# Performance work log

Hardware: AMD Instinct MI355X
Metric: run time of the kernel (lower is better)

Reference implementation:

```python
import jax, jax.numpy as jnp
import numpy as np

B, T, C = 2, 2048, 2048
N_HEAD, D_HEAD = 16, 128

def setup_inputs() -> dict:
    key = jax.random.key(0)
    k1, k2, k3 = jax.random.split(key, 3)
    x = jax.random.normal(k1, (B, T, C), dtype=jnp.float32)
    # lecun-normal-ish scaling for kernels
    W_attn = jax.random.normal(k2, (C, 3 * C), dtype=jnp.float32) * (1.0 / np.sqrt(C))
    W_proj = jax.random.normal(k3, (C, C), dtype=jnp.float32) * (1.0 / np.sqrt(C))
    return {"x": x, "W_attn": W_attn, "W_proj": W_proj}

def reference(x, W_attn, W_proj):
    Bx, Tx, Cx = x.shape
    # fused qkv projection: (B,T,C) @ (C,3C)
    qkv = x @ W_attn
    q, k, v = jnp.split(qkv, 3, axis=-1)
    # (B, H, T, Dh)
    q = q.reshape(Bx, Tx, N_HEAD, D_HEAD).transpose(0, 2, 1, 3)
    k = k.reshape(Bx, Tx, N_HEAD, D_HEAD).transpose(0, 2, 1, 3)
    v = v.reshape(Bx, Tx, N_HEAD, D_HEAD).transpose(0, 2, 1, 3)
    scale = 1.0 / jnp.sqrt(jnp.asarray(D_HEAD, dtype=x.dtype))
    att = jnp.einsum('bhqd,bhkd->bhqk', q, k) * scale  # (B,H,T,T)
    causal_mask = jnp.tril(jnp.ones((Tx, Tx), dtype=jnp.bool_))[None, None]
    att = jnp.where(causal_mask, att, -jnp.inf)
    att = jax.nn.softmax(att, axis=-1)
    y = jnp.einsum('bhqk,bhkd->bhqd', att, v)
    y = y.transpose(0, 2, 1, 3).reshape(Bx, Tx, Cx)
    return y @ W_proj
```

## Files before the change

kernel.cpp:

```cpp
#include <hip/hip_runtime.h>
#include <hip/hip_bf16.h>
#include <stdint.h>

#define AS1 __attribute__((address_space(1)))
#define AS3 __attribute__((address_space(3)))

typedef __bf16 bf16_t;
typedef __bf16 bf16x8 __attribute__((ext_vector_type(8)));
typedef float f32x4 __attribute__((ext_vector_type(4)));
typedef float f32x16 __attribute__((ext_vector_type(16)));

static constexpr int Bsz = 2, T = 2048, Cdim = 2048, NH = 16, DH = 128;
static constexpr int M  = Bsz * T;
static constexpr int N1 = 3 * Cdim;
static constexpr int K1 = Cdim;

__device__ __forceinline__ unsigned short f2bf(float f) {
  unsigned u = __float_as_uint(f);
  u += 0x7fffu + ((u >> 16) & 1u);
  return (unsigned short)(u >> 16);
}

__device__ __forceinline__ void gload_lds16(const bf16_t* g, void* l) {
  __builtin_amdgcn_global_load_lds((AS1 const void*)g, (AS3 void*)l, 16, 0, 0);
}

__device__ __forceinline__ float ex2(float x) {
  float r; asm("v_exp_f32 %0, %1" : "=v"(r) : "v"(x)); return r;
}
__device__ __forceinline__ unsigned pk2(float a, float b) {
  unsigned r; asm("v_cvt_pk_bf16_f32 %0, %1, %2" : "=v"(r) : "v"(a), "v"(b)); return r;
}

__global__ __launch_bounds__(256) void preamble_kernel(const float* __restrict__ x,
                                                       const float* __restrict__ Wa,
                                                       const float* __restrict__ Wp,
                                                       unsigned short* __restrict__ xb,
                                                       unsigned short* __restrict__ WaT,
                                                       unsigned short* __restrict__ WpT) {
  __shared__ float tile[32][33];
  const int blk = blockIdx.x;
  const int tid = threadIdx.x;
  if (blk < 8192) {
    int i = blk * 1024 + tid * 4;
    float4 v = *(const float4*)(x + i);
    ushort4 o;
    o.x = f2bf(v.x); o.y = f2bf(v.y); o.z = f2bf(v.z); o.w = f2bf(v.w);
    *(ushort4*)(xb + i) = o;
    return;
  }
  const float* in;
  unsigned short* out;
  int Nn, bi;
  if (blk < 20480) { in = Wa; out = WaT; Nn = N1;   bi = blk - 8192;  }
  else             { in = Wp; out = WpT; Nn = Cdim; bi = blk - 20480; }
  const int ntiles = Nn >> 5;
  const int n0 = (bi % ntiles) * 32, k0 = (bi / ntiles) * 32;
  const int tx = tid & 31, ty = tid >> 5;
#pragma unroll
  for (int i = 0; i < 32; i += 8)
    tile[ty + i][tx] = in[(size_t)(k0 + ty + i) * Nn + n0 + tx];
  __syncthreads();
#pragma unroll
  for (int i = 0; i < 32; i += 8)
    out[(size_t)(n0 + ty + i) * K1 + k0 + tx] = f2bf(tile[tx][ty + i]);
}

__global__ __launch_bounds__(512, 2) void gemm_q(const bf16_t* __restrict__ A,
                                                 const bf16_t* __restrict__ BT,
                                                 void* __restrict__ Cp,
                                                 int Nn, int Kk) {
  constexpr int SLOT = 32768;
  __shared__ __align__(16) char ldsmem[3 * SLOT];
  char* ldsb = ldsmem;

  const int tid = threadIdx.x;
  const int lane = tid & 63;
  const int wid = tid >> 6;
  const int lq = lane & 15, lk = lane >> 4;
  const int wr = wid >> 2, wc = wid & 3;

  const int bid = blockIdx.x;
  const int xcd = bid & 7;
  const int j = bid >> 3;
  const int r = j & 15, s5 = j >> 4;
  const int tn = s5 * 8 + (r & 7);
  const int tm = xcd * 2 + (r >> 3);

  f32x4 acc[8][4] = {};

  int aoff[8], boff[4];
#pragma unroll
  for (int m = 0; m < 8; ++m) {
    int row = wr * 128 + m * 16 + lq;
    aoff[m] = row * 64 + ((lk * 16) ^ (((row >> 1) & 3) << 4));
  }
#pragma unroll
  for (int n = 0; n < 4; ++n) {
    int brow = wc * 64 + n * 16 + lq;
    boff[n] = 16384 + brow * 64 + ((lk * 16) ^ (((brow >> 1) & 3) << 4));
  }

  const int pA0 = tid * 16;
  const int ar0 = pA0 >> 6;
  const int ac0 = (pA0 & 63) ^ (((ar0 >> 1) & 3) << 4);
  const bf16_t* Ags0 = A + (size_t)(tm * 256 + ar0) * Kk + (ac0 >> 1);
  const int pA1 = 8192 + tid * 16;
  const int ar1 = pA1 >> 6;
  const int ac1 = (pA1 & 63) ^ (((ar1 >> 1) & 3) << 4);
  const bf16_t* Ags1 = A + (size_t)(tm * 256 + ar1) * Kk + (ac1 >> 1);
  const bf16_t* Bgs0 = BT + (size_t)(tn * 256 + ar0) * Kk + (ac0 >> 1);
  const bf16_t* Bgs1 = BT + (size_t)(tn * 256 + ar1) * Kk + (ac1 >> 1);

  auto stage = [&](int kt, int slot) {
    char* db = ldsb + slot * SLOT;
    gload_lds16(Ags0 + (size_t)kt * 32, db + tid * 16);
    gload_lds16(Ags1 + (size_t)kt * 32, db + 8192 + tid * 16);
    gload_lds16(Bgs0 + (size_t)kt * 32, db + 16384 + tid * 16);
    gload_lds16(Bgs1 + (size_t)kt * 32, db + 24576 + tid * 16);
  };

  const int nk = Kk >> 5;

  stage(0, 0); stage(1, 1);
  asm volatile("s_waitcnt vmcnt(4)" ::: "memory");
  __builtin_amdgcn_s_barrier();

#define QTILE(KT, SLOT0, SLOT2, STAGE_EN, VM)                                    \
  {                                                                              \
    const char* sb = ldsb + (SLOT0) * SLOT;                                      \
    bf16x8 af[8], bfv[4];                                                        \
    _Pragma("unroll") for (int m = 0; m < 8; ++m)                                \
      af[m] = *(const bf16x8*)(sb + aoff[m]);                                    \
    _Pragma("unroll") for (int n = 0; n < 4; ++n)                                \
      bfv[n] = *(const bf16x8*)(sb + boff[n]);                                   \
    if (STAGE_EN) stage((KT) + 2, (SLOT2));                                      \
    _Pragma("unroll") for (int m = 0; m < 8; ++m)                                \
      _Pragma("unroll") for (int n = 0; n < 4; ++n)                              \
        acc[m][n] =                                                              \
            __builtin_amdgcn_mfma_f32_16x16x32_bf16(af[m], bfv[n], acc[m][n], 0, 0, 0); \
    asm volatile("s_waitcnt vmcnt(" #VM ")" ::: "memory");                       \
    __builtin_amdgcn_s_barrier();                                                \
  }

  {
    int c0 = 0;
    for (int kt = 0; kt < nk - 2; ++kt) {
      const int c2 = (c0 >= 1) ? (c0 - 1) : (c0 + 2);
      QTILE(kt, c0, c2, 1, 4);
      c0 = (c0 >= 2) ? 0 : (c0 + 1);
    }
    QTILE(nk - 2, c0, 0, 0, 0);
    c0 = (c0 >= 2) ? 0 : (c0 + 1);
    QTILE(nk - 1, c0, 0, 0, 0);
  }
#undef QTILE

  if (tn >= 16) {
    unsigned short* q16 = (unsigned short*)Cp;
#pragma unroll
    for (int m = 0; m < 8; ++m)
#pragma unroll
      for (int n = 0; n < 4; ++n) {
        int row = tm * 256 + wr * 128 + m * 16 + lk * 4;
        int b_ = row >> 11, t0 = row & 2047;
        int c = tn * 256 - 4096 + wc * 64 + n * 16 + lq;
        ushort4 o;
        o.x = f2bf(acc[m][n][0]); o.y = f2bf(acc[m][n][1]);
        o.z = f2bf(acc[m][n][2]); o.w = f2bf(acc[m][n][3]);
        *(ushort4*)(q16 + (size_t)(b_ * 2048 + c) * N1 + 4096 + t0) = o;
      }
  } else {
#pragma unroll
    for (int m = 0; m < 8; ++m)
#pragma unroll
      for (int n = 0; n < 4; ++n)
#pragma unroll
        for (int r2 = 0; r2 < 4; ++r2) {
          int row = tm * 256 + wr * 128 + m * 16 + lk * 4 + r2;
          int col = tn * 256 + wc * 64 + n * 16 + lq;
          ((unsigned short*)Cp)[(size_t)row * Nn + col] = f2bf(acc[m][n][r2]);
        }
  }
}

template <int MODE>
__global__ __launch_bounds__(512, 4) void gemm_p3(const bf16_t* __restrict__ A,
                                                  const bf16_t* __restrict__ BT,
                                                  void* __restrict__ Cp,
                                                  int Nn, int Kk) {
  constexpr int SLOT = 24576;
  __shared__ __align__(16) char ldsmem[3 * SLOT];
  char* ldsb = ldsmem;

  const int tid = threadIdx.x;
  const int wid = tid >> 6, lane = tid & 63;
  const int lq = lane & 15, lk = lane >> 4;
  const int wr = wid >> 2, wc = wid & 3;

  const int bid = blockIdx.x;
  const int xcd = bid & 7;
  const int j = bid >> 3;
  const int r = j & 31, s5 = j >> 5;
  const int tn = s5 * 8 + (r & 7);
  const int tm = xcd * 4 + (r >> 3);

  f32x4 acc[4][4] = {};

  int aoff[4], boff[4];
#pragma unroll
  for (int m = 0; m < 4; ++m) {
    int row = wr * 64 + m * 16 + lq;
    aoff[m] = row * 64 + ((lk * 16) ^ (((row >> 1) & 3) << 4));
  }
#pragma unroll
  for (int n = 0; n < 4; ++n) {
    int brow = wc * 64 + n * 16 + lq;
    boff[n] = 8192 + brow * 64 + ((lk * 16) ^ (((brow >> 1) & 3) << 4));
  }

  const int pA = wid * 1024 + lane * 16;
  const int arow = pA >> 6;
  const int acsw = (pA & 63) ^ (((arow >> 1) & 3) << 4);
  const bf16_t* Ags = A + (size_t)(tm * 128 + arow) * Kk + (acsw >> 1);

  const int pB0 = wid * 1024 + lane * 16;
  const int brow0 = pB0 >> 6;
  const int bcsw0 = (pB0 & 63) ^ (((brow0 >> 1) & 3) << 4);
  const bf16_t* Bgs0 = BT + (size_t)(tn * 256 + brow0) * Kk + (bcsw0 >> 1);

  const int pB1 = 8192 + wid * 1024 + lane * 16;
  const int brow1 = pB1 >> 6;
  const int bcsw1 = (pB1 & 63) ^ (((brow1 >> 1) & 3) << 4);
  const bf16_t* Bgs1 = BT + (size_t)(tn * 256 + brow1) * Kk + (bcsw1 >> 1);

  const int ldsA = wid * 1024;
  const int ldsB0 = 8192 + wid * 1024;
  const int ldsB1 = 16384 + wid * 1024;

  auto stage = [&](int kt, int slot) {
    char* db = ldsb + slot * SLOT;
    gload_lds16(Ags + (size_t)kt * 32, db + ldsA);
    gload_lds16(Bgs0 + (size_t)kt * 32, db + ldsB0);
    gload_lds16(Bgs1 + (size_t)kt * 32, db + ldsB1);
  };

  const int nk = Kk >> 5;

  stage(0, 0); stage(1, 1);
  asm volatile("s_waitcnt vmcnt(3)" ::: "memory");
  __builtin_amdgcn_s_barrier();

#define TILE_BODY(KT, SLOT0, SLOT2, STAGE_EN, VM)                                \
  {                                                                              \
    __builtin_amdgcn_sched_barrier(0);                                           \
    const char* sb = ldsb + (SLOT0) * SLOT;                                      \
    bf16x8 af[4], bfv[4];                                                        \
    _Pragma("unroll") for (int m = 0; m < 4; ++m)                                \
      af[m] = *(const bf16x8*)(sb + aoff[m]);                                    \
    _Pragma("unroll") for (int n = 0; n < 4; ++n)                                \
      bfv[n] = *(const bf16x8*)(sb + boff[n]);                                   \
    if (STAGE_EN) stage((KT) + 2, (SLOT2));                                      \
    __builtin_amdgcn_sched_barrier(0);                                           \
    __builtin_amdgcn_s_barrier();                                                \
    asm volatile("s_waitcnt lgkmcnt(0)" ::: "memory");                           \
    __builtin_amdgcn_sched_barrier(0);                                           \
    __builtin_amdgcn_s_setprio(1);                                               \
    _Pragma("unroll") for (int m = 0; m < 4; ++m)                                \
      _Pragma("unroll") for (int n = 0; n < 4; ++n)                              \
        acc[m][n] =                                                              \
            __builtin_amdgcn_mfma_f32_16x16x32_bf16(af[m], bfv[n], acc[m][n], 0, 0, 0); \
    __builtin_amdgcn_s_setprio(0);                                               \
    __builtin_amdgcn_sched_barrier(0);                                           \
    asm volatile("s_waitcnt vmcnt(" #VM ")" ::: "memory");                       \
    __builtin_amdgcn_s_barrier();                                                \
  }

  {
    int c0 = 0;
    for (int kt = 0; kt < nk - 2; ++kt) {
      const int c2 = (c0 >= 1) ? (c0 - 1) : (c0 + 2);
      TILE_BODY(kt, c0, c2, 1, 3);
      c0 = (c0 >= 2) ? 0 : (c0 + 1);
    }
    TILE_BODY(nk - 2, c0, 0, 0, 0);
    c0 = (c0 >= 2) ? 0 : (c0 + 1);
    TILE_BODY(nk - 1, c0, 0, 0, 0);
  }
#undef TILE_BODY

#pragma unroll
  for (int m = 0; m < 4; ++m)
#pragma unroll
    for (int n = 0; n < 4; ++n)
#pragma unroll
      for (int r2 = 0; r2 < 4; ++r2) {
        int row = tm * 128 + wr * 64 + m * 16 + lk * 4 + r2;
        int col = tn * 256 + wc * 64 + n * 16 + lq;
        if (MODE == 1)
          ((unsigned short*)Cp)[(size_t)row * Nn + col] = f2bf(acc[m][n][r2]);
        else
          ((float*)Cp)[(size_t)row * Nn + col] = acc[m][n][r2];
      }
}

__global__ __launch_bounds__(512, 1) void attn_kernel(const bf16_t* __restrict__ qkv,
                                                      unsigned short* __restrict__ y) {
  __shared__ __align__(16) char lds[98304];
  const int tid = threadIdx.x;
  const int wid = tid >> 6, lane = tid & 63;
  const int l31 = lane & 31, hi = lane >> 5;
  const int hi16 = hi << 4;
  const int bh = blockIdx.x;
  const int g = blockIdx.y;
  const int b = bh >> 4, h = bh & 15;
  const float SC2 = 0.12751879868954096f;

  const int grp = (wid < 4) ? g : (15 - g);
  const int qlo = grp * 128 + (wid & 3) * 32;
  const int qidx = qlo + l31;
  const int nt = 2 * (15 - g) + 2;
  const size_t rowbase = (size_t)(b * T) * N1;

  bf16x8 qf[8];
  {
    const bf16_t* Qg = qkv + rowbase + (size_t)qidx * N1 + h * DH + hi * 8;
#pragma unroll
    for (int kk = 0; kk < 8; ++kk) qf[kk] = *(const bf16x8*)(Qg + kk * 16);
  }

  const bf16_t* Kg0 = qkv + rowbase + Cdim + h * DH;
  const bf16_t* Vg0 = qkv + (size_t)(b * 2048 + h * DH) * N1 + 2 * Cdim;
  const int p0 = wid * 1024 + lane * 16;
  const int p1 = 8192 + wid * 1024 + lane * 16;
  const int kr0 = p0 >> 8, kr1 = p1 >> 8;
  const bf16_t* KsA = Kg0 + (size_t)kr0 * N1 + ((((p0 & 255) ^ ((kr0 & 15) << 4))) >> 1);
  const bf16_t* KsB = Kg0 + (size_t)kr1 * N1 + ((((p1 & 255) ^ ((kr1 & 15) << 4))) >> 1);
  const int vr0 = p0 >> 7, vr1 = p1 >> 7;
  const bf16_t* VsA = Vg0 + (size_t)vr0 * N1 + ((((p0 & 127) ^ ((vr0 & 7) << 4))) >> 1);
  const bf16_t* VsB = Vg0 + (size_t)vr1 * N1 + ((((p1 & 127) ^ ((vr1 & 7) << 4))) >> 1);
  const int dstoff = wid * 1024;

  auto stage = [&](int tt, int slot) {
    char* Kd = lds + slot * 32768;
    char* Vd = Kd + 16384;
    const size_t ko = (size_t)(tt * 64) * N1;
    const int vo = tt * 64;
    gload_lds16(KsA + ko, Kd + dstoff);
    gload_lds16(KsB + ko, Kd + 8192 + dstoff);
    gload_lds16(VsA + vo, Vd + dstoff);
    gload_lds16(VsB + vo, Vd + 8192 + dstoff);
  };

  f32x16 oacc[4] = {};
  float mrow = -1e30f, lrow = 0.f;

  stage(0, 0); stage(1, 1);
  asm volatile("s_waitcnt vmcnt(4)" ::: "memory");
  __builtin_amdgcn_s_barrier();

  int cs = 0;
  for (int t = 0; t < nt; ++t) {
    const int kv0 = t * 64;
    if (t + 2 < nt) {
      const int s2 = (cs >= 1) ? (cs - 1) : (cs + 2);
      stage(t + 2, s2);
    }

    if (kv0 <= qlo + 31) {
      f32x16 s0 = {}, s1 = {};
      {
        const char* Kb = lds + cs * 32768;
        const char* krow0 = Kb + l31 * 256;
        const char* krow1 = Kb + (32 + l31) * 256;
        const int sw0 = (l31 & 15) << 4;
#pragma unroll
        for (int kk = 0; kk < 8; ++kk) {
          bf16x8 kf0 = *(const bf16x8*)(krow0 + ((kk * 32 + hi16) ^ sw0));
          bf16x8 kf1 = *(const bf16x8*)(krow1 + ((kk * 32 + hi16) ^ sw0));
          s0 = __builtin_amdgcn_mfma_f32_32x32x16_bf16(kf0, qf[kk], s0, 0, 0, 0);
          s1 = __builtin_amdgcn_mfma_f32_32x32x16_bf16(kf1, qf[kk], s1, 0, 0, 0);
        }
      }
      float sv[32];
#pragma unroll
      for (int r = 0; r < 16; ++r) { sv[r] = s0[r]; sv[16 + r] = s1[r]; }
      if (kv0 + 63 > qlo) {
#pragma unroll
        for (int r = 0; r < 16; ++r) {
          const int roff = (r & 3) + 8 * (r >> 2);
          if (kv0 + roff + 4 * hi > qidx) sv[r] = -1e30f;
          if (kv0 + 32 + roff + 4 * hi > qidx) sv[16 + r] = -1e30f;
        }
      }
      float mx = sv[0];
#pragma unroll
      for (int i = 1; i < 32; ++i) mx = fmaxf(mx, sv[i]);
      mx = fmaxf(mx, __shfl_xor(mx, 32));
      const float mn = fmaxf(mrow, mx);
      const float osc = ex2((mrow - mn) * SC2);
      mrow = mn;
      const float mn2 = mn * SC2;
#pragma unroll
      for (int db = 0; db < 4; ++db) oacc[db] *= osc;
      float srow = 0.f;
#pragma unroll
      for (int i = 0; i < 32; ++i) {
        float p = ex2(fmaf(sv[i], SC2, -mn2));
        sv[i] = p;
        srow += p;
      }
      srow += __shfl_xor(srow, 32);
      lrow = lrow * osc + srow;
      bf16x8 pb[4];
#pragma unroll
      for (int s4 = 0; s4 < 4; ++s4) {
        const int base = (s4 >> 1) * 16 + (s4 & 1) * 8;
        unsigned x0 = pk2(sv[base + 0], sv[base + 1]);
        unsigned x1 = pk2(sv[base + 2], sv[base + 3]);
        unsigned y0 = pk2(sv[base + 4], sv[base + 5]);
        unsigned y1 = pk2(sv[base + 6], sv[base + 7]);
        unsigned e0 = (unsigned)__shfl_xor((int)(hi ? x0 : y0), 32);
        unsigned e1 = (unsigned)__shfl_xor((int)(hi ? x1 : y1), 32);
        union { unsigned u[4]; bf16x8 v; } pbu;
        pbu.u[0] = hi ? e0 : x0;
        pbu.u[1] = hi ? e1 : x1;
        pbu.u[2] = hi ? y0 : e0;
        pbu.u[3] = hi ? y1 : e1;
        pb[s4] = pbu.v;
      }
      {
        const char* Vb = lds + cs * 32768 + 16384;
#pragma unroll
        for (int db = 0; db < 4; ++db) {
          const int vrow = db * 32 + l31;
          const char* vr = Vb + vrow * 128;
          const int swv = (vrow & 7) << 4;
#pragma unroll
          for (int s4 = 0; s4 < 4; ++s4) {
            bf16x8 vf = *(const bf16x8*)(vr + ((s4 * 32 + hi16) ^ swv));
            oacc[db] = __builtin_amdgcn_mfma_f32_32x32x16_bf16(vf, pb[s4], oacc[db], 0, 0, 0);
          }
        }
      }
    }

    asm volatile("s_waitcnt vmcnt(4)" ::: "memory");
    __builtin_amdgcn_s_barrier();
    cs = (cs >= 2) ? 0 : (cs + 1);
  }

  const float inv = 1.0f / lrow;
  char* eb = lds + wid * 8192;
#pragma unroll
  for (int db = 0; db < 4; ++db)
#pragma unroll
    for (int r = 0; r < 16; ++r) {
      const int d = db * 32 + (r & 3) + 8 * (r >> 2) + 4 * hi;
      const int off = l31 * 256 + ((d * 2) ^ ((l31 & 15) << 4));
      *(unsigned short*)(eb + off) = f2bf(oacc[db][r] * inv);
    }
  asm volatile("s_waitcnt lgkmcnt(0)" ::: "memory");
  __builtin_amdgcn_sched_barrier(0);
  {
    unsigned short* yr = y + (size_t)(b * T + qlo + l31) * Cdim + h * DH;
#pragma unroll
    for (int rr = 0; rr < 8; ++rr) {
      const int c = hi * 8 + rr;
      bf16x8 v = *(const bf16x8*)(eb + l31 * 256 + ((c * 16) ^ ((l31 & 15) << 4)));
      *(bf16x8*)(yr + c * 8) = v;
    }
  }
}

extern "C" void kernel_launch(void* const* d_in, const int* in_sizes, int n_in,
                              void* d_out, int out_size, void* d_ws, size_t ws_size,
                              hipStream_t stream) {
  const float* x  = (const float*)d_in[0];
  const float* Wa = (const float*)d_in[1];
  const float* Wp = (const float*)d_in[2];
  float* out = (float*)d_out;
  char* ws = (char*)d_ws;

  size_t o0 = 0;
  size_t o1 = o0 + (size_t)M * K1 * 2;
  size_t o2 = o1 + (size_t)N1 * K1 * 2;
  size_t o3 = o2 + (size_t)M * N1 * 2;
  size_t o4 = o3 + (size_t)M * Cdim * 2;

  unsigned short* xb   = (unsigned short*)(ws + o0);
  unsigned short* WaT  = (unsigned short*)(ws + o1);
  unsigned short* qkvb = (unsigned short*)(ws + o2);
  unsigned short* yb   = (unsigned short*)(ws + o3);
  unsigned short* WpT  = (unsigned short*)(ws + o4);

  preamble_kernel<<<dim3(24576), dim3(256), 0, stream>>>(x, Wa, Wp, xb, WaT, WpT);

  gemm_q<<<dim3((M / 256) * (N1 / 256)), dim3(512), 0, stream>>>(
      (const bf16_t*)xb, (const bf16_t*)WaT, (void*)qkvb, N1, K1);

  attn_kernel<<<dim3(Bsz * NH, 8), dim3(512), 0, stream>>>(
      (const bf16_t*)qkvb, yb);

  gemm_p3<0><<<dim3((M / 128) * (Cdim / 256)), dim3(512), 0, stream>>>(
      (const bf16_t*)yb, (const bf16_t*)WpT, (void*)out, Cdim, K1);
}
```

Before: 238.7 us.

## Deepen QKV GEMM pipeline to four LDS stages and simplify projection GEMM scheduling

The QKV GEMM moves from a 3-slot to a 4-slot LDS ring buffer, prefetching three k-tiles ahead. It drops occupancy from 2 to 1 block per CU to make room for the 128KB of LDS, trading latency hiding across blocks for deeper in-block prefetch. The projection GEMM becomes a non-template float-output kernel. Its sched_barrier, extra s_barrier, lgkmcnt wait and setprio scheduling hints are removed, leaving the compiler to schedule the LDS reads and MFMAs.

```diff
diff --git a/kernel.cpp b/kernel.cpp
--- a/kernel.cpp
+++ b/kernel.cpp
@@ -66,12 +66,12 @@
     out[(size_t)(n0 + ty + i) * K1 + k0 + tx] = f2bf(tile[tx][ty + i]);
 }
 
-__global__ __launch_bounds__(512, 2) void gemm_q(const bf16_t* __restrict__ A,
+__global__ __launch_bounds__(512, 1) void gemm_q(const bf16_t* __restrict__ A,
                                                  const bf16_t* __restrict__ BT,
                                                  void* __restrict__ Cp,
                                                  int Nn, int Kk) {
   constexpr int SLOT = 32768;
-  __shared__ __align__(16) char ldsmem[3 * SLOT];
+  __shared__ __align__(16) char ldsmem[4 * SLOT];
   char* ldsb = ldsmem;
 
   const int tid = threadIdx.x;
@@ -122,11 +122,11 @@
 
   const int nk = Kk >> 5;
 
-  stage(0, 0); stage(1, 1);
-  asm volatile("s_waitcnt vmcnt(4)" ::: "memory");
+  stage(0, 0); stage(1, 1); stage(2, 2);
+  asm volatile("s_waitcnt vmcnt(8)" ::: "memory");
   __builtin_amdgcn_s_barrier();
 
-#define QTILE(KT, SLOT0, SLOT2, STAGE_EN, VM)                                    \
+#define QTILE(KT, SLOT0, SLOT3, STAGE_EN, VM)                                    \
   {                                                                              \
     const char* sb = ldsb + (SLOT0) * SLOT;                                      \
     bf16x8 af[8], bfv[4];                                                        \
@@ -134,7 +134,7 @@
       af[m] = *(const bf16x8*)(sb + aoff[m]);                                    \
     _Pragma("unroll") for (int n = 0; n < 4; ++n)                                \
       bfv[n] = *(const bf16x8*)(sb + boff[n]);                                   \
-    if (STAGE_EN) stage((KT) + 2, (SLOT2));                                      \
+    if (STAGE_EN) stage((KT) + 3, (SLOT3));                                      \
     _Pragma("unroll") for (int m = 0; m < 8; ++m)                                \
       _Pragma("unroll") for (int n = 0; n < 4; ++n)                              \
         acc[m][n] =                                                              \
@@ -145,13 +145,15 @@
 
   {
     int c0 = 0;
-    for (int kt = 0; kt < nk - 2; ++kt) {
-      const int c2 = (c0 >= 1) ? (c0 - 1) : (c0 + 2);
-      QTILE(kt, c0, c2, 1, 4);
-      c0 = (c0 >= 2) ? 0 : (c0 + 1);
-    }
+    for (int kt = 0; kt < nk - 3; ++kt) {
+      const int c3 = (c0 + 3) & 3;
+      QTILE(kt, c0, c3, 1, 8);
+      c0 = (c0 + 1) & 3;
+    }
+    QTILE(nk - 3, c0, 0, 0, 4);
+    c0 = (c0 + 1) & 3;
     QTILE(nk - 2, c0, 0, 0, 0);
-    c0 = (c0 >= 2) ? 0 : (c0 + 1);
+    c0 = (c0 + 1) & 3;
     QTILE(nk - 1, c0, 0, 0, 0);
   }
 #undef QTILE
@@ -184,11 +186,10 @@
   }
 }
 
-template <int MODE>
-__global__ __launch_bounds__(512, 4) void gemm_p3(const bf16_t* __restrict__ A,
-                                                  const bf16_t* __restrict__ BT,
-                                                  void* __restrict__ Cp,
-                                                  int Nn, int Kk) {
+__global__ __launch_bounds__(512, 4) void gemm_s(const bf16_t* __restrict__ A,
+                                                 const bf16_t* __restrict__ BT,
+                                                 float* __restrict__ Cp,
+                                                 int Nn, int Kk) {
   constexpr int SLOT = 24576;
   __shared__ __align__(16) char ldsmem[3 * SLOT];
   char* ldsb = ldsmem;
@@ -251,9 +252,8 @@
   asm volatile("s_waitcnt vmcnt(3)" ::: "memory");
   __builtin_amdgcn_s_barrier();
 
-#define TILE_BODY(KT, SLOT0, SLOT2, STAGE_EN, VM)                                \
+#define STILE(KT, SLOT0, SLOT2, STAGE_EN, VM)                                    \
   {                                                                              \
-    __builtin_amdgcn_sched_barrier(0);                                           \
     const char* sb = ldsb + (SLOT0) * SLOT;                                      \
     bf16x8 af[4], bfv[4];                                                        \
     _Pragma("unroll") for (int m = 0; m < 4; ++m)                                \
@@ -261,17 +261,10 @@
     _Pragma("unroll") for (int n = 0; n < 4; ++n)                                \
       bfv[n] = *(const bf16x8*)(sb + boff[n]);                                   \
     if (STAGE_EN) stage((KT) + 2, (SLOT2));                                      \
-    __builtin_amdgcn_sched_barrier(0);                                           \
-    __builtin_amdgcn_s_barrier();                                                \
-    asm volatile("s_waitcnt lgkmcnt(0)" ::: "memory");                           \
-    __builtin_amdgcn_sched_barrier(0);                                           \
-    __builtin_amdgcn_s_setprio(1);                                               \
     _Pragma("unroll") for (int m = 0; m < 4; ++m)                                \
       _Pragma("unroll") for (int n = 0; n < 4; ++n)                              \
         acc[m][n] =                                                              \
             __builtin_amdgcn_mfma_f32_16x16x32_bf16(af[m], bfv[n], acc[m][n], 0, 0, 0); \
-    __builtin_amdgcn_s_setprio(0);                                               \
-    __builtin_amdgcn_sched_barrier(0);                                           \
     asm volatile("s_waitcnt vmcnt(" #VM ")" ::: "memory");                       \
     __builtin_amdgcn_s_barrier();                                                \
   }
@@ -280,14 +273,14 @@
     int c0 = 0;
     for (int kt = 0; kt < nk - 2; ++kt) {
       const int c2 = (c0 >= 1) ? (c0 - 1) : (c0 + 2);
-      TILE_BODY(kt, c0, c2, 1, 3);
+      STILE(kt, c0, c2, 1, 3);
       c0 = (c0 >= 2) ? 0 : (c0 + 1);
     }
-    TILE_BODY(nk - 2, c0, 0, 0, 0);
+    STILE(nk - 2, c0, 0, 0, 0);
     c0 = (c0 >= 2) ? 0 : (c0 + 1);
-    TILE_BODY(nk - 1, c0, 0, 0, 0);
-  }
-#undef TILE_BODY
+    STILE(nk - 1, c0, 0, 0, 0);
+  }
+#undef STILE
 
 #pragma unroll
   for (int m = 0; m < 4; ++m)
@@ -297,10 +290,7 @@
       for (int r2 = 0; r2 < 4; ++r2) {
         int row = tm * 128 + wr * 64 + m * 16 + lk * 4 + r2;
         int col = tn * 256 + wc * 64 + n * 16 + lq;
-        if (MODE == 1)
-          ((unsigned short*)Cp)[(size_t)row * Nn + col] = f2bf(acc[m][n][r2]);
-        else
-          ((float*)Cp)[(size_t)row * Nn + col] = acc[m][n][r2];
+        Cp[(size_t)row * Nn + col] = acc[m][n][r2];
       }
 }
 
@@ -502,6 +492,6 @@
   attn_kernel<<<dim3(Bsz * NH, 8), dim3(512), 0, stream>>>(
       (const bf16_t*)qkvb, yb);
 
-  gemm_p3<0><<<dim3((M / 128) * (Cdim / 256)), dim3(512), 0, stream>>>(
-      (const bf16_t*)yb, (const bf16_t*)WpT, (void*)out, Cdim, K1);
-}
+  gemm_s<<<dim3((M / 128) * (Cdim / 256)), dim3(512), 0, stream>>>(
+      (const bf16_t*)yb, (const bf16_t*)WpT, out, Cdim, K1);
+}
```

Result: no change. 236.7 us (-0.9%).
